# Optimization experiments

Hardware: AMD Instinct MI355X
Metric: run time of the kernel (lower is better)

## Reference

```python
import jax, jax.numpy as jnp
import numpy as np

B, N1, N2, DIM1, DIM2, DK = 4, 4096, 2048, 256, 256, 256


def setup_inputs() -> dict:
    key = jax.random.key(0)
    ks = jax.random.split(key, 8)
    s1 = 1.0 / np.sqrt(DIM2)  # torch Linear default init scale (uniform bound)
    s2 = 1.0 / np.sqrt(DIM1)
    return {
        "x1": jax.random.normal(ks[0], (B, N1, DIM1), jnp.float32),
        "x2": jax.random.normal(ks[1], (B, N2, DIM2), jnp.float32),
        "WQ": jax.random.uniform(ks[2], (DK, DIM2), jnp.float32, -s1, s1),
        "bQ": jax.random.uniform(ks[3], (DK,), jnp.float32, -s1, s1),
        "WK": jax.random.uniform(ks[4], (DK, DIM1), jnp.float32, -s2, s2),
        "bK": jax.random.uniform(ks[5], (DK,), jnp.float32, -s2, s2),
        "WV": jax.random.uniform(ks[6], (DK, DIM1), jnp.float32, -s2, s2),
        "bV": jax.random.uniform(ks[7], (DK,), jnp.float32, -s2, s2),
    }


def reference(x1, x2, WQ, bQ, WK, bK, WV, bV):
    # Projections (torch Linear: x @ W^T + b)
    Q = jnp.einsum('bnd,kd->bnk', x2, WQ) + bQ  # [B, N2, DK]
    K = jnp.einsum('bmd,kd->bmk', x1, WK) + bK  # [B, N1, DK]
    V = jnp.einsum('bmd,kd->bmk', x1, WV) + bV  # [B, N1, DK]

    QK = jnp.einsum('bnk,bmk->bnm', Q, K)                          # [B, N2, N1]
    P = (jnp.einsum('bnk,bmk->bnm', jnp.tanh(Q), jnp.tanh(K)) + 1.0) * 0.5
    scores = QK * P / jnp.sqrt(jnp.float32(DK))
    attn = jax.nn.softmax(scores, axis=-1)                         # [B, N2, N1]
    Q_hat = jnp.einsum('bnm,bmk->bnk', attn, V)                    # [B, N2, DK]
    return (Q, Q_hat, attn)
```

## Files before the change

### kernel.cpp

```cpp
#include <hip/hip_runtime.h>
#include <hip/hip_bf16.h>

typedef __bf16 bf16;
typedef __bf16 bf16x4 __attribute__((ext_vector_type(4)));
typedef __bf16 bf16x8 __attribute__((ext_vector_type(8)));
typedef float  f32x4  __attribute__((ext_vector_type(4)));

#define DEVI static __device__ __forceinline__

constexpr int NB = 4;
constexpr int N1 = 4096;
constexpr int N2 = 2048;
constexpr int D  = 256;

DEVI f32x4 mfma16(bf16x8 a, bf16x8 b, f32x4 c) {
  return __builtin_amdgcn_mfma_f32_16x16x32_bf16(a, b, c, 0, 0, 0);
}

typedef const __attribute__((address_space(1))) void* gas_t;
typedef __attribute__((address_space(3))) void* las_t;

DEVI void gload_lds16(const void* g, void* l) {
  __builtin_amdgcn_global_load_lds((gas_t)g, (las_t)l, 16, 0, 0);
}

DEVI void fence_sched() { __builtin_amdgcn_sched_barrier(0); }

__global__ __launch_bounds__(256)
void projQ_kernel(const float* __restrict__ A, const float* __restrict__ Bm,
                  const float* __restrict__ bias,
                  float* __restrict__ outF, bf16* __restrict__ out1,
                  bf16* __restrict__ out2)
{
  __shared__ bf16 Ah[128][64], Al[128][64];
  __shared__ bf16 Bh[64][64],  Bl[64][64];
  const int tid  = threadIdx.x;
  const int lane = tid & 63, wid = tid >> 6;
  const int wr = wid >> 1, wc = wid & 1;
  const int m0 = blockIdx.x * 128, n0 = blockIdx.y * 64;

  f32x4 acc[4][2];
#pragma unroll
  for (int i = 0; i < 4; ++i)
#pragma unroll
    for (int j = 0; j < 2; ++j) acc[i][j] = f32x4{0.f, 0.f, 0.f, 0.f};

  for (int kt = 0; kt < 4; ++kt) {
    const int k0 = kt * 64;
    if (kt) __syncthreads();
#pragma unroll
    for (int i = 0; i < 8; ++i) {
      int idx = i * 256 + tid;
      int r = idx >> 4, c4 = idx & 15;
      const float4 v = *(const float4*)(A + (size_t)(m0 + r) * D + k0 + c4 * 4);
      bf16x4 h, l;
      h[0] = (bf16)v.x; h[1] = (bf16)v.y; h[2] = (bf16)v.z; h[3] = (bf16)v.w;
      l[0] = (bf16)(v.x - (float)h[0]); l[1] = (bf16)(v.y - (float)h[1]);
      l[2] = (bf16)(v.z - (float)h[2]); l[3] = (bf16)(v.w - (float)h[3]);
      *(bf16x4*)&Ah[r][c4 * 4] = h;
      *(bf16x4*)&Al[r][c4 * 4] = l;
    }
#pragma unroll
    for (int i = 0; i < 4; ++i) {
      int idx = i * 256 + tid;
      int r = idx >> 4, c4 = idx & 15;
      const float4 v = *(const float4*)(Bm + (size_t)(n0 + r) * D + k0 + c4 * 4);
      bf16x4 h, l;
      h[0] = (bf16)v.x; h[1] = (bf16)v.y; h[2] = (bf16)v.z; h[3] = (bf16)v.w;
      l[0] = (bf16)(v.x - (float)h[0]); l[1] = (bf16)(v.y - (float)h[1]);
      l[2] = (bf16)(v.z - (float)h[2]); l[3] = (bf16)(v.w - (float)h[3]);
      *(bf16x4*)&Bh[r][c4 * 4] = h;
      *(bf16x4*)&Bl[r][c4 * 4] = l;
    }
    __syncthreads();
#pragma unroll
    for (int kc = 0; kc < 2; ++kc) {
      const int ko = kc * 32 + (lane >> 4) * 8;
      bf16x8 ah[4], al[4];
#pragma unroll
      for (int mf = 0; mf < 4; ++mf) {
        ah[mf] = *(bf16x8*)&Ah[wr * 64 + mf * 16 + (lane & 15)][ko];
        al[mf] = *(bf16x8*)&Al[wr * 64 + mf * 16 + (lane & 15)][ko];
      }
#pragma unroll
      for (int nf = 0; nf < 2; ++nf) {
        bf16x8 bh = *(bf16x8*)&Bh[wc * 32 + nf * 16 + (lane & 15)][ko];
        bf16x8 bl = *(bf16x8*)&Bl[wc * 32 + nf * 16 + (lane & 15)][ko];
#pragma unroll
        for (int mf = 0; mf < 4; ++mf) {
          acc[mf][nf] = mfma16(ah[mf], bh, acc[mf][nf]);
          acc[mf][nf] = mfma16(ah[mf], bl, acc[mf][nf]);
          acc[mf][nf] = mfma16(al[mf], bh, acc[mf][nf]);
        }
      }
    }
  }

#pragma unroll
  for (int nf = 0; nf < 2; ++nf) {
    const int col = n0 + wc * 32 + nf * 16 + (lane & 15);
    const float bcol = bias[col];
#pragma unroll
    for (int mf = 0; mf < 4; ++mf) {
#pragma unroll
      for (int r = 0; r < 4; ++r) {
        const int row = m0 + wr * 64 + mf * 16 + (lane >> 4) * 4 + r;
        float v = acc[mf][nf][r] + bcol;
        outF[(size_t)row * D + col] = v;
        out1[(size_t)row * D + col] = (bf16)v;
        out2[(size_t)row * D + col] = (bf16)tanhf(v);
      }
    }
  }
}

template<int MODE>
__global__ __launch_bounds__(256)
void proj_kernel(const float* __restrict__ A, const float* __restrict__ Bm,
                 const float* __restrict__ bias,
                 bf16* __restrict__ out1, bf16* __restrict__ out2)
{
  __shared__ bf16 As[128][64];
  __shared__ bf16 Bs[64][64];
  const int tid  = threadIdx.x;
  const int lane = tid & 63, wid = tid >> 6;
  const int wr = wid >> 1, wc = wid & 1;
  const int m0 = blockIdx.x * 128, n0 = blockIdx.y * 64;

  f32x4 acc[4][2];
#pragma unroll
  for (int i = 0; i < 4; ++i)
#pragma unroll
    for (int j = 0; j < 2; ++j) acc[i][j] = f32x4{0.f, 0.f, 0.f, 0.f};

  for (int kt = 0; kt < 4; ++kt) {
    const int k0 = kt * 64;
    if (kt) __syncthreads();
#pragma unroll
    for (int i = 0; i < 8; ++i) {
      int idx = i * 256 + tid;
      int r = idx >> 4, c4 = idx & 15;
      const float4 v = *(const float4*)(A + (size_t)(m0 + r) * D + k0 + c4 * 4);
      bf16x4 bv; bv[0] = (bf16)v.x; bv[1] = (bf16)v.y; bv[2] = (bf16)v.z; bv[3] = (bf16)v.w;
      *(bf16x4*)&As[r][c4 * 4] = bv;
    }
#pragma unroll
    for (int i = 0; i < 4; ++i) {
      int idx = i * 256 + tid;
      int r = idx >> 4, c4 = idx & 15;
      const float4 v = *(const float4*)(Bm + (size_t)(n0 + r) * D + k0 + c4 * 4);
      bf16x4 bv; bv[0] = (bf16)v.x; bv[1] = (bf16)v.y; bv[2] = (bf16)v.z; bv[3] = (bf16)v.w;
      *(bf16x4*)&Bs[r][c4 * 4] = bv;
    }
    __syncthreads();
#pragma unroll
    for (int kc = 0; kc < 2; ++kc) {
      const int ko = kc * 32 + (lane >> 4) * 8;
      bf16x8 a[4];
#pragma unroll
      for (int mf = 0; mf < 4; ++mf)
        a[mf] = *(bf16x8*)&As[wr * 64 + mf * 16 + (lane & 15)][ko];
#pragma unroll
      for (int nf = 0; nf < 2; ++nf) {
        bf16x8 bb = *(bf16x8*)&Bs[wc * 32 + nf * 16 + (lane & 15)][ko];
#pragma unroll
        for (int mf = 0; mf < 4; ++mf) acc[mf][nf] = mfma16(a[mf], bb, acc[mf][nf]);
      }
    }
  }

#pragma unroll
  for (int nf = 0; nf < 2; ++nf) {
    const int col = n0 + wc * 32 + nf * 16 + (lane & 15);
    float bcol = 0.f;
    if constexpr (MODE == 1) bcol = bias[col];
#pragma unroll
    for (int mf = 0; mf < 4; ++mf) {
#pragma unroll
      for (int r = 0; r < 4; ++r) {
        const int row = m0 + wr * 64 + mf * 16 + (lane >> 4) * 4 + r;
        float v = acc[mf][nf][r];
        if constexpr (MODE == 1) {
          v += bcol;
          out1[(size_t)row * D + col] = (bf16)v;
          out2[(size_t)row * D + col] = (bf16)tanhf(v);
        } else {
          v += bias[row];
          out1[(size_t)(col >> 12) * (D * N1) + (size_t)row * N1 + (col & 4095)] = (bf16)v;
        }
      }
    }
  }
}

__global__ __launch_bounds__(512, 4)
void scores_kernel(const bf16* __restrict__ Qb, const bf16* __restrict__ tQb,
                   const bf16* __restrict__ Kb, const bf16* __restrict__ tKb,
                   bf16* __restrict__ E, float* __restrict__ partials)
{
  __shared__ bf16 SM[2][4][128][32];
  __shared__ float rowpart[128][4];
  const int tid = threadIdx.x, lane = tid & 63, wid = tid >> 6;
  const int wr = wid >> 2;
  const int wc = wid & 3;
  const int lo16 = lane & 15, hi = lane >> 4;
  const int mt = blockIdx.x, nt = blockIdx.y, b = blockIdx.z;
  const int RQ = b * N2 + nt * 128;
  const int RK = b * N1 + mt * 128;

  f32x4 accS[4][2], accP[4][2];
#pragma unroll
  for (int i = 0; i < 4; ++i)
#pragma unroll
    for (int j = 0; j < 2; ++j) {
      accS[i][j] = f32x4{0.f, 0.f, 0.f, 0.f};
      accP[i][j] = f32x4{0.f, 0.f, 0.f, 0.f};
    }

  const int srow = tid >> 2;
  const int scol = ((tid & 3) ^ ((srow >> 1) & 3)) << 3;

  auto stage = [&](int kt, int buf) {
    const int col = kt * 32 + scol;
    char* base = (char*)&SM[buf][0][0][0] + tid * 16;
    gload_lds16(Qb  + (size_t)(RQ + srow) * D + col, base);
    gload_lds16(tQb + (size_t)(RQ + srow) * D + col, base + 8192);
    gload_lds16(Kb  + (size_t)(RK + srow) * D + col, base + 16384);
    gload_lds16(tKb + (size_t)(RK + srow) * D + col, base + 24576);
  };

  auto cpt = [&](int buf) {
    bf16x8 aS[4], aT[4];
#pragma unroll
    for (int mf = 0; mf < 4; ++mf) {
      const int row = wr * 64 + mf * 16 + lo16;
      const int ko = (hi ^ ((row >> 1) & 3)) << 3;
      aS[mf] = *(bf16x8*)&SM[buf][0][row][ko];
      aT[mf] = *(bf16x8*)&SM[buf][1][row][ko];
    }
#pragma unroll
    for (int nf = 0; nf < 2; ++nf) {
      const int row = wc * 32 + nf * 16 + lo16;
      const int ko = (hi ^ ((row >> 1) & 3)) << 3;
      bf16x8 bS = *(bf16x8*)&SM[buf][2][row][ko];
      bf16x8 bT = *(bf16x8*)&SM[buf][3][row][ko];
#pragma unroll
      for (int mf = 0; mf < 4; ++mf) {
        accS[mf][nf] = mfma16(aS[mf], bS, accS[mf][nf]);
        accP[mf][nf] = mfma16(aT[mf], bT, accP[mf][nf]);
      }
    }
  };

  stage(0, 0);
  fence_sched();
  int cur = 0;
#pragma unroll
  for (int kt = 0; kt < 8; ++kt) {
    if (kt < 7) {
      stage(kt + 1, cur ^ 1);
      fence_sched();
      asm volatile("s_waitcnt vmcnt(4)\n\ts_barrier" ::: "memory");
    } else {
      asm volatile("s_waitcnt vmcnt(0)\n\ts_barrier" ::: "memory");
    }
    cpt(cur);
    asm volatile("s_barrier" ::: "memory");
    cur ^= 1;
  }

#pragma unroll
  for (int mf = 0; mf < 4; ++mf) {
    f32x4 rs = f32x4{0.f, 0.f, 0.f, 0.f};
#pragma unroll
    for (int nf = 0; nf < 2; ++nf) {
      const int m_g = mt * 128 + wc * 32 + nf * 16 + lo16;
#pragma unroll
      for (int r = 0; r < 4; ++r) {
        const int n_g = b * N2 + nt * 128 + wr * 64 + mf * 16 + hi * 4 + r;
        float s = accS[mf][nf][r] * (accP[mf][nf][r] + 1.0f) * 0.03125f;
        float e = __expf(s);
        E[(size_t)n_g * N1 + m_g] = (bf16)e;
        rs[r] += e;
      }
    }
#pragma unroll
    for (int r = 0; r < 4; ++r) {
      float v = rs[r];
      v += __shfl_xor(v, 1); v += __shfl_xor(v, 2);
      v += __shfl_xor(v, 4); v += __shfl_xor(v, 8);
      if (lo16 == 0)
        rowpart[wr * 64 + mf * 16 + hi * 4 + r][wc] = v;
    }
  }
  __syncthreads();
  if (tid < 128) {
    float p = rowpart[tid][0] + rowpart[tid][1] + rowpart[tid][2] + rowpart[tid][3];
    partials[(size_t)(b * N2 + nt * 128 + tid) * 32 + mt] = p;
  }
}

__global__ __launch_bounds__(256)
void rowsum_kernel(const float* __restrict__ partials, float* __restrict__ rinv)
{
  int r = blockIdx.x * 256 + threadIdx.x;
  const float* pr = partials + (size_t)r * 32;
  f32x4 s4 = *(const f32x4*)pr;
#pragma unroll
  for (int j = 1; j < 8; ++j) s4 += *(const f32x4*)(pr + j * 4);
  rinv[r] = 1.0f / (s4[0] + s4[1] + s4[2] + s4[3]);
}

__global__ __launch_bounds__(512)
void qhat_kernel(const bf16* __restrict__ E, const bf16* __restrict__ Vt,
                 const float* __restrict__ partials,
                 float* __restrict__ attn, bf16* __restrict__ partQ)
{
  __shared__ bf16 Es[2][128][64];
  __shared__ bf16 Vs[2][256][64];
  __shared__ float rowinv[128];
  const int tid = threadIdx.x, lane = tid & 63, wid = tid >> 6;
  const int lo16 = lane & 15, hi = lane >> 4;
  const int wr = wid & 3;
  const int wh = wid >> 2;
  const int n0 = blockIdx.x * 128;
  const int q  = blockIdx.y;
  const int b  = blockIdx.z;
  const int mq = q * 1024;
  const size_t nbase = (size_t)b * N2 + n0;
  const bf16* vb = Vt + (size_t)b * (D * N1) + mq;

  if (tid < 128) {
    const float* pr = partials + (nbase + tid) * 32;
    f32x4 s4 = *(const f32x4*)pr;
#pragma unroll
    for (int j = 1; j < 8; ++j) s4 += *(const f32x4*)(pr + j * 4);
    rowinv[tid] = 1.0f / (s4[0] + s4[1] + s4[2] + s4[3]);
  }

  auto stage = [&](int ms, int buf) {
#pragma unroll
    for (int i = 0; i < 2; ++i) {
      const int c = i * 512 + tid;
      const int row = c >> 3;
      const int lg = (c & 7) ^ (row & 7);
      gload_lds16(E + (nbase + row) * N1 + mq + ms * 64 + lg * 8,
                  (char*)&Es[buf][0][0] + c * 16);
    }
#pragma unroll
    for (int i = 0; i < 4; ++i) {
      const int c = i * 512 + tid;
      const int row = c >> 3;
      const int lg = (c & 7) ^ (row & 7);
      gload_lds16(vb + (size_t)row * N1 + ms * 64 + lg * 8,
                  (char*)&Vs[buf][0][0] + c * 16);
    }
  };

  f32x4 acc[2][8];
#pragma unroll
  for (int i = 0; i < 2; ++i)
#pragma unroll
    for (int j = 0; j < 8; ++j) acc[i][j] = f32x4{0.f, 0.f, 0.f, 0.f};

  auto cpt = [&](int buf) {
#pragma unroll
    for (int kc = 0; kc < 2; ++kc) {
      bf16x8 a[2];
#pragma unroll
      for (int mf = 0; mf < 2; ++mf) {
        const int row = wr * 32 + mf * 16 + lo16;
        const int ph = (kc * 4 + hi) ^ (row & 7);
        a[mf] = *(bf16x8*)((char*)&Es[buf][0][0] + row * 128 + ph * 16);
      }
#pragma unroll
      for (int nf = 0; nf < 8; ++nf) {
        const int row = wh * 128 + nf * 16 + lo16;
        const int ph = (kc * 4 + hi) ^ (row & 7);
        bf16x8 bb = *(bf16x8*)((char*)&Vs[buf][0][0] + row * 128 + ph * 16);
        acc[0][nf] = mfma16(a[0], bb, acc[0][nf]);
        acc[1][nf] = mfma16(a[1], bb, acc[1][nf]);
      }
    }
  };

  auto attnwrite = [&](int ms, int buf) {
#pragma unroll
    for (int i = 0; i < 2; ++i) {
      const int c = i * 512 + tid;
      const int row = c >> 3;
      const int lg = (c & 7) ^ (row & 7);
      bf16x8 ev = *(bf16x8*)((char*)&Es[buf][0][0] + c * 16);
      const float inv = rowinv[row];
      float v[8];
#pragma unroll
      for (int j = 0; j < 8; ++j) v[j] = (float)ev[j] * inv;
      float* dst = attn + (nbase + row) * N1 + mq + ms * 64 + lg * 8;
      float4 w0 = {v[0], v[1], v[2], v[3]};
      float4 w1 = {v[4], v[5], v[6], v[7]};
      *(float4*)(dst)     = w0;
      *(float4*)(dst + 4) = w1;
    }
  };

  stage(0, 0);
  fence_sched();
  __syncthreads();

  int buf = 0;
  for (int ms = 0; ms < 16; ++ms) {
    if (ms < 15) { stage(ms + 1, buf ^ 1); fence_sched(); }
    if (ms == 0)
      asm volatile("s_waitcnt vmcnt(6)\n\ts_barrier" ::: "memory");
    else if (ms < 15)
      asm volatile("s_waitcnt vmcnt(10)\n\ts_barrier" ::: "memory");
    else
      asm volatile("s_waitcnt vmcnt(4)\n\ts_barrier" ::: "memory");
    cpt(buf);
    attnwrite(ms, buf);
    asm volatile("s_barrier" ::: "memory");
    buf ^= 1;
  }

#pragma unroll
  for (int mf = 0; mf < 2; ++mf)
#pragma unroll
    for (int nf = 0; nf < 8; ++nf)
#pragma unroll
      for (int r = 0; r < 4; ++r) {
        const int n  = n0 + wr * 32 + mf * 16 + hi * 4 + r;
        const int dk = wh * 128 + nf * 16 + lo16;
        partQ[((size_t)(q * NB + b) * N2 + n) * D + dk] = (bf16)acc[mf][nf][r];
      }
}

__global__ __launch_bounds__(256)
void reduceQ_kernel(const bf16* __restrict__ P, const float* __restrict__ rinv,
                    float* __restrict__ Qhat)
{
  const size_t t  = (size_t)blockIdx.x * 256 + threadIdx.x;
  const size_t rn = t >> 5;
  const int    ch = (int)(t & 31);
  const size_t base = rn * 256 + ch * 8;
  const size_t S = (size_t)NB * N2 * D;
  bf16x8 p0 = *(const bf16x8*)(P + base);
  bf16x8 p1 = *(const bf16x8*)(P + S + base);
  bf16x8 p2 = *(const bf16x8*)(P + 2 * S + base);
  bf16x8 p3 = *(const bf16x8*)(P + 3 * S + base);
  const float inv = rinv[rn];
  float o[8];
#pragma unroll
  for (int j = 0; j < 8; ++j)
    o[j] = (((float)p0[j] + (float)p1[j]) + ((float)p2[j] + (float)p3[j])) * inv;
  float4 w0 = {o[0], o[1], o[2], o[3]};
  float4 w1 = {o[4], o[5], o[6], o[7]};
  *(float4*)(Qhat + base)     = w0;
  *(float4*)(Qhat + base + 4) = w1;
}

extern "C" void kernel_launch(void* const* d_in, const int* in_sizes, int n_in,
                              void* d_out, int out_size, void* d_ws, size_t ws_size,
                              hipStream_t stream)
{
  const float* x1 = (const float*)d_in[0];
  const float* x2 = (const float*)d_in[1];
  const float* WQ = (const float*)d_in[2];
  const float* bQ = (const float*)d_in[3];
  const float* WK = (const float*)d_in[4];
  const float* bK = (const float*)d_in[5];
  const float* WV = (const float*)d_in[6];
  const float* bV = (const float*)d_in[7];

  float* out  = (float*)d_out;
  float* Qf   = out;
  float* Qhat = out + 2097152;
  float* attn = out + 4194304;

  char* ws = (char*)d_ws;
  bf16* Qb   = (bf16*)(ws + (0ull  << 20));
  bf16* tQb  = (bf16*)(ws + (4ull  << 20));
  bf16* Kb   = (bf16*)(ws + (8ull  << 20));
  bf16* tKb  = (bf16*)(ws + (16ull << 20));
  bf16* Vt   = (bf16*)(ws + (24ull << 20));
  bf16* E    = (bf16*)(ws + (32ull << 20));
  float* partials = (float*)(ws + (96ull << 20));
  float* rinv     = (float*)(ws + (98ull << 20));
  bf16*  partQ    = (bf16*)(ws + (100ull << 20));

  projQ_kernel    <<<dim3(64, 4),   256, 0, stream>>>(x2, WQ, bQ, Qf, Qb, tQb);
  proj_kernel<1>  <<<dim3(128, 4),  256, 0, stream>>>(x1, WK, bK, Kb, tKb);
  proj_kernel<2>  <<<dim3(2, 256),  256, 0, stream>>>(WV, x1, bV, Vt, nullptr);
  scores_kernel   <<<dim3(32, 16, 4), 512, 0, stream>>>(Qb, tQb, Kb, tKb, E, partials);
  rowsum_kernel   <<<32, 256, 0, stream>>>(partials, rinv);
  qhat_kernel     <<<dim3(16, 4, 4), 512, 0, stream>>>(E, Vt, partials, attn, partQ);
  reduceQ_kernel  <<<1024, 256, 0, stream>>>(partQ, rinv, Qhat);
}
```

Before: 173.4 us.

## Drop rowsum kernel, remap qhat blocks per XCD, raise MFMA wave priority

Removes the separate rowsum launch by having reduceQ compute each row's inverse sum directly from the partials with a wave shuffle reduction. Remaps qhat's 1D grid so that all blocks sharing a (q,b) slab of V land on the same XCD, improving L2 reuse of V. Wraps the MFMA compute phases in s_setprio so compute waves are favoured over memory waves. The qhat change trades the 3D grid for manual index decoding that depends on round-robin XCD dispatch.

```diff
diff --git a/kernel.cpp b/kernel.cpp
--- a/kernel.cpp
+++ b/kernel.cpp
@@ -264,7 +264,9 @@
     } else {
       asm volatile("s_waitcnt vmcnt(0)\n\ts_barrier" ::: "memory");
     }
+    __builtin_amdgcn_s_setprio(1);
     cpt(cur);
+    __builtin_amdgcn_s_setprio(0);
     asm volatile("s_barrier" ::: "memory");
     cur ^= 1;
   }
@@ -298,17 +300,6 @@
     float p = rowpart[tid][0] + rowpart[tid][1] + rowpart[tid][2] + rowpart[tid][3];
     partials[(size_t)(b * N2 + nt * 128 + tid) * 32 + mt] = p;
   }
-}
-
-__global__ __launch_bounds__(256)
-void rowsum_kernel(const float* __restrict__ partials, float* __restrict__ rinv)
-{
-  int r = blockIdx.x * 256 + threadIdx.x;
-  const float* pr = partials + (size_t)r * 32;
-  f32x4 s4 = *(const f32x4*)pr;
-#pragma unroll
-  for (int j = 1; j < 8; ++j) s4 += *(const f32x4*)(pr + j * 4);
-  rinv[r] = 1.0f / (s4[0] + s4[1] + s4[2] + s4[3]);
 }
 
 __global__ __launch_bounds__(512)
@@ -323,9 +314,14 @@
   const int lo16 = lane & 15, hi = lane >> 4;
   const int wr = wid & 3;
   const int wh = wid >> 2;
-  const int n0 = blockIdx.x * 128;
-  const int q  = blockIdx.y;
-  const int b  = blockIdx.z;
+  const int wgid = blockIdx.x;
+  const int xcd  = wgid & 7;
+  const int slot = wgid >> 3;
+  const int combo = xcd * 2 + (slot >> 4);
+  const int nt = slot & 15;
+  const int q  = combo >> 2;
+  const int b  = combo & 3;
+  const int n0 = nt * 128;
   const int mq = q * 1024;
   const size_t nbase = (size_t)b * N2 + n0;
   const bf16* vb = Vt + (size_t)b * (D * N1) + mq;
@@ -416,7 +412,9 @@
       asm volatile("s_waitcnt vmcnt(10)\n\ts_barrier" ::: "memory");
     else
       asm volatile("s_waitcnt vmcnt(4)\n\ts_barrier" ::: "memory");
+    __builtin_amdgcn_s_setprio(1);
     cpt(buf);
+    __builtin_amdgcn_s_setprio(0);
     attnwrite(ms, buf);
     asm volatile("s_barrier" ::: "memory");
     buf ^= 1;
@@ -435,23 +433,27 @@
 }
 
 __global__ __launch_bounds__(256)
-void reduceQ_kernel(const bf16* __restrict__ P, const float* __restrict__ rinv,
+void reduceQ_kernel(const bf16* __restrict__ P, const float* __restrict__ partials,
                     float* __restrict__ Qhat)
 {
-  const size_t t  = (size_t)blockIdx.x * 256 + threadIdx.x;
-  const size_t rn = t >> 5;
-  const int    ch = (int)(t & 31);
-  const size_t base = rn * 256 + ch * 8;
+  const int tid = threadIdx.x;
+  const size_t rn = (size_t)blockIdx.x * 8 + (tid >> 5);
+  const int j = tid & 31;
+  float s = partials[rn * 32 + j];
+  s += __shfl_xor(s, 1); s += __shfl_xor(s, 2); s += __shfl_xor(s, 4);
+  s += __shfl_xor(s, 8); s += __shfl_xor(s, 16);
+  const float inv = 1.0f / s;
+
+  const size_t base = rn * 256 + (size_t)j * 8;
   const size_t S = (size_t)NB * N2 * D;
   bf16x8 p0 = *(const bf16x8*)(P + base);
   bf16x8 p1 = *(const bf16x8*)(P + S + base);
   bf16x8 p2 = *(const bf16x8*)(P + 2 * S + base);
   bf16x8 p3 = *(const bf16x8*)(P + 3 * S + base);
-  const float inv = rinv[rn];
   float o[8];
 #pragma unroll
-  for (int j = 0; j < 8; ++j)
-    o[j] = (((float)p0[j] + (float)p1[j]) + ((float)p2[j] + (float)p3[j])) * inv;
+  for (int jj = 0; jj < 8; ++jj)
+    o[jj] = (((float)p0[jj] + (float)p1[jj]) + ((float)p2[jj] + (float)p3[jj])) * inv;
   float4 w0 = {o[0], o[1], o[2], o[3]};
   float4 w1 = {o[4], o[5], o[6], o[7]};
   *(float4*)(Qhat + base)     = w0;
@@ -484,14 +486,12 @@
   bf16* Vt   = (bf16*)(ws + (24ull << 20));
   bf16* E    = (bf16*)(ws + (32ull << 20));
   float* partials = (float*)(ws + (96ull << 20));
-  float* rinv     = (float*)(ws + (98ull << 20));
   bf16*  partQ    = (bf16*)(ws + (100ull << 20));
 
   projQ_kernel    <<<dim3(64, 4),   256, 0, stream>>>(x2, WQ, bQ, Qf, Qb, tQb);
   proj_kernel<1>  <<<dim3(128, 4),  256, 0, stream>>>(x1, WK, bK, Kb, tKb);
   proj_kernel<2>  <<<dim3(2, 256),  256, 0, stream>>>(WV, x1, bV, Vt, nullptr);
   scores_kernel   <<<dim3(32, 16, 4), 512, 0, stream>>>(Qb, tQb, Kb, tKb, E, partials);
-  rowsum_kernel   <<<32, 256, 0, stream>>>(partials, rinv);
-  qhat_kernel     <<<dim3(16, 4, 4), 512, 0, stream>>>(E, Vt, partials, attn, partQ);
-  reduceQ_kernel  <<<1024, 256, 0, stream>>>(partQ, rinv, Qhat);
-}
+  qhat_kernel     <<<256, 512, 0, stream>>>(E, Vt, partials, attn, partQ);
+  reduceQ_kernel  <<<1024, 256, 0, stream>>>(partQ, partials, Qhat);
+}
```

Measured after the change: 171.7 us. No clear change (-1.0%).
